# Kernel optimization log

Measured on AMD Instinct MI355X. Metric: run time of the kernel, lower is better.

The kernel has to match this reference:

```python
import jax, jax.numpy as jnp
import numpy as np

TAU = 2.0      # spikingjelly LIF default membrane time constant
VTH = 1.0      # threshold
SCALE = 0.25
NUM_HEADS = 16
EPS = 1e-5


def lif(x):
    # single-step LIF from rest (v=0, v_reset=0): u = v + (x - v)/tau = x/tau; spike = H(u - vth)
    return (x / TAU >= VTH).astype(x.dtype)


def bn(z, gamma, beta, mean, var):
    # inference-mode BatchNorm1d over channel dim of (TB, C, N)
    inv = gamma / jnp.sqrt(var + EPS)
    return z * inv[:, None] + (beta - mean * inv)[:, None]


def branch(z, w, gamma, beta, mean, var):
    # conv1x1 (pointwise channel mix) -> BN -> LIF
    z = jnp.einsum('oc,bcn->bon', w, z)
    return lif(bn(z, gamma, beta, mean, var))


def setup_inputs() -> dict:
    key = jax.random.key(0)
    ks = jax.random.split(key, 8)
    T, B, C, N = 4, 2, 512, 512
    x = jax.random.normal(ks[0], (T, B, C, N), dtype=jnp.float32)
    y = jax.random.normal(ks[1], (T, B, C, N), dtype=jnp.float32)
    def conv_w(k):
        return jax.random.normal(k, (C, C), dtype=jnp.float32) / np.float32(np.sqrt(C))
    def bn_params(k):
        km, kv = jax.random.split(k)
        gamma = jnp.full((C,), 2.0, dtype=jnp.float32)  # scale so LIF spikes are non-trivially sparse
        beta = jnp.zeros((C,), dtype=jnp.float32)
        mean = 0.1 * jax.random.normal(km, (C,), dtype=jnp.float32)
        var = 0.5 + jax.random.uniform(kv, (C,), dtype=jnp.float32)
        return gamma, beta, mean, var
    q_g, q_b, q_m, q_v = bn_params(ks[2])
    k_g, k_b, k_m, k_v = bn_params(ks[3])
    v_g, v_b, v_m, v_v = bn_params(ks[4])
    p_g, p_b, p_m, p_v = bn_params(ks[5])
    return {
        'x': x, 'y': y,
        'q_w': conv_w(jax.random.fold_in(key, 10)), 'q_g': q_g, 'q_b': q_b, 'q_m': q_m, 'q_v': q_v,
        'k_w': conv_w(jax.random.fold_in(key, 11)), 'k_g': k_g, 'k_b': k_b, 'k_m': k_m, 'k_v': k_v,
        'v_w': conv_w(jax.random.fold_in(key, 12)), 'v_g': v_g, 'v_b': v_b, 'v_m': v_m, 'v_v': v_v,
        'p_w': conv_w(jax.random.fold_in(key, 13)), 'p_g': p_g, 'p_b': p_b, 'p_m': p_m, 'p_v': p_v,
    }


def reference(x, y, q_w, q_g, q_b, q_m, q_v, k_w, k_g, k_b, k_m, k_v,
              v_w, v_g, v_b, v_m, v_v, p_w, p_g, p_b, p_m, p_v):
    T, B, C, N = x.shape
    H = NUM_HEADS
    D = C // H
    xq = x.reshape(T * B, C, N)
    yk = y.reshape(T * B, C, N)
    # q/k/v: conv1x1 + BN + LIF, then split heads: (T,B,C,N) -> (T,B,H,N,D)
    q = branch(xq, q_w, q_g, q_b, q_m, q_v).reshape(T, B, H, D, N).transpose(0, 1, 2, 4, 3)
    k = branch(yk, k_w, k_g, k_b, k_m, k_v).reshape(T, B, H, D, N).transpose(0, 1, 2, 4, 3)
    v = branch(yk, v_w, v_g, v_b, v_m, v_v).reshape(T, B, H, D, N).transpose(0, 1, 2, 4, 3)
    # softmax-free spiking attention: (Q K^T) V * scale
    attn = jnp.einsum('tbhnd,tbhmd->tbhnm', q, k)
    o = jnp.einsum('tbhnm,tbhmd->tbhnd', attn, v) * SCALE
    o = o.transpose(0, 1, 2, 4, 3).reshape(T, B, C, N)  # (T,B,H,D,N) -> (T,B,C,N)
    o = lif(o.reshape(T * B, C, N))
    o = branch(o, p_w, p_g, p_b, p_m, p_v).reshape(T, B, C, N)
    return o
```

## Files before the change

kernel.cpp:

```cpp
#include <hip/hip_runtime.h>
#include <math.h>

#define TBD 8
#define CD  512
#define ND  512
#define PLANE (TBD*CD*ND)
#define WPL   (CD*CD)

typedef unsigned short u16;
typedef unsigned int u32;
typedef _Float16 f16;
typedef __attribute__((ext_vector_type(8))) short bf16x8;
typedef __attribute__((ext_vector_type(8))) _Float16 f16x8;
typedef __attribute__((ext_vector_type(4))) float f32x4;

__device__ __forceinline__ float b2f(u16 u){
  union{u32 i; float f;} x; x.i = ((u32)u) << 16; return x.f;
}
__device__ __forceinline__ u16 f2b(float f){
  u32 u = __builtin_bit_cast(u32, f);
  u += 0x7fffu + ((u >> 16) & 1u);
  return (u16)(u >> 16);
}
__device__ __forceinline__ void async_ld16(const void* g, void* l){
  __builtin_amdgcn_global_load_lds((const __attribute__((address_space(1))) u32*)g,
      (__attribute__((address_space(3))) u32*)l, 16, 0, 0);
}

__global__ __launch_bounds__(256) void prep(
    const float* __restrict__ x, const float* __restrict__ y,
    const float* __restrict__ Qw, const float* __restrict__ Kw,
    const float* __restrict__ Vw, const float* __restrict__ Pw,
    const float* __restrict__ Qg, const float* __restrict__ Qb, const float* __restrict__ Qm, const float* __restrict__ Qv,
    const float* __restrict__ Kg, const float* __restrict__ Kb, const float* __restrict__ Km, const float* __restrict__ Kv,
    const float* __restrict__ Vg, const float* __restrict__ Vb, const float* __restrict__ Vm, const float* __restrict__ Vv,
    const float* __restrict__ Pg, const float* __restrict__ Pb, const float* __restrict__ Pm, const float* __restrict__ Pv,
    u16* __restrict__ wsu, float* __restrict__ ib)
{
  const int bx = blockIdx.x, t = threadIdx.x;
  if (bx < 1024) {
    __shared__ __align__(16) float tl[64][68];
    const int inp = bx >> 9, rem = bx & 511;
    const int tb = rem >> 6, tile = rem & 63;
    const int ct = (tile & 7) << 6, nt = (tile >> 3) << 6;
    const float* xg = inp ? y : x;
    #pragma unroll
    for (int r = 0; r < 4; ++r) {
      const int row = (t >> 4) + (r << 4);
      const int col = (t & 15) << 2;
      *(float4*)&tl[row][col] =
          *(const float4*)(xg + ((size_t)(tb*CD + ct + row))*ND + nt + col);
    }
    __syncthreads();
    const int nl = t >> 2, cb = (t & 3) << 4;
    __align__(16) u16 h[3][16];
    #pragma unroll
    for (int j = 0; j < 16; ++j) {
      const float f = tl[cb + j][nl];
      const u16 a = f2b(f);  const float r1 = f - b2f(a);
      const u16 b = f2b(r1); const float r2 = r1 - b2f(b);
      h[0][j] = a; h[1][j] = b; h[2][j] = f2b(r2);
    }
    u16* base = wsu + (size_t)inp*3*PLANE;
    const size_t rowo = ((size_t)tb*ND + nt + nl)*CD + ct + cb;
    #pragma unroll
    for (int s = 0; s < 3; ++s) {
      *(uint4*)(base + (size_t)s*PLANE + rowo)     = *(uint4*)&h[s][0];
      *(uint4*)(base + (size_t)s*PLANE + rowo + 8) = *(uint4*)&h[s][8];
    }
  } else if (bx < 2048) {
    const int b2 = bx - 1024;
    const int mat = b2 >> 8, rr = b2 & 255;
    const float* Wg = (mat==0)?Qw:(mat==1)?Kw:(mat==2)?Vw:Pw;
    const int row = (rr << 1) + (t >> 7);
    const int col = (t & 127) << 2;
    const float4 w = *(const float4*)(Wg + (size_t)row*CD + col);
    const float f[4] = {w.x, w.y, w.z, w.w};
    __align__(8) u16 h[3][4];
    #pragma unroll
    for (int j = 0; j < 4; ++j) {
      const u16 a = f2b(f[j]);  const float r1 = f[j] - b2f(a);
      const u16 b = f2b(r1);    const float r2 = r1 - b2f(b);
      h[0][j] = a; h[1][j] = b; h[2][j] = f2b(r2);
    }
    u16* base = wsu + (size_t)6*PLANE + (size_t)mat*3*WPL;
    #pragma unroll
    for (int s = 0; s < 3; ++s)
      *(uint2*)(base + (size_t)s*WPL + (size_t)row*CD + col) = *(uint2*)&h[s][0];
  } else {
    const int idx = (bx - 2048)*256 + t;
    const int br = idx >> 9, ch = idx & 511;
    const float* G = (br==0)?Qg:(br==1)?Kg:(br==2)?Vg:Pg;
    const float* B = (br==0)?Qb:(br==1)?Kb:(br==2)?Vb:Pb;
    const float* M = (br==0)?Qm:(br==1)?Km:(br==2)?Vm:Pm;
    const float* V = (br==0)?Qv:(br==1)?Kv:(br==2)?Vv:Pv;
    const float inv = G[ch] / sqrtf(V[ch] + 1e-5f);
    ib[br*1024 + ch]       = inv;
    ib[br*1024 + 512 + ch] = B[ch] - M[ch]*inv;
  }
}

template<int XS>
__global__ __launch_bounds__(256) void gemm_mfma(
    const u16* __restrict__ Ab, const u16* __restrict__ Bbp,
    const float* __restrict__ ibp,
    u16* __restrict__ qt, u16* __restrict__ spk, float* __restrict__ outf)
{
  const int bx  = blockIdx.x;
  const int idx = bx & 511;
  const int br  = bx >> 9;
  const int tb  = idx & 7;
  const int o0  = ((idx >> 3) & 7) << 6;
  const int n0  = (idx >> 6) << 6;
  const int t    = threadIdx.x;
  const int lane = t & 63, wave = t >> 6;

  const u16* A = Ab + (size_t)br*3*WPL;
  const u16* B = Bbp + (size_t)(br ? 3 : 0)*PLANE;
  const float* IB = ibp + br*1024;

  __shared__ __align__(16) u16 smem[2*3*4*512 + 2*XS*4*512];
  u16* Al = smem;
  u16* Bl = smem + 2*3*4*512;

  const int lr = lane >> 2;
  const int lc = ((lane & 3) ^ ((lane >> 3) & 3)) << 3;
  constexpr int TPW = (12 + 4*XS) / 4;

  auto stage = [&](int buf, int c0) {
    #pragma unroll
    for (int j = 0; j < TPW; ++j) {
      const int tix = wave*TPW + j;
      if (tix < 12) {
        const int s = tix >> 2, ot = tix & 3;
        async_ld16(A + (size_t)s*WPL + (size_t)(o0 + (ot<<4) + lr)*CD + c0 + lc,
                   Al + (((buf*3 + s)*4 + ot) << 9) + (lane << 3));
      } else {
        const int k = tix - 12, s = k >> 2, nt = k & 3;
        async_ld16(B + (size_t)s*PLANE + ((size_t)tb*ND + n0 + (nt<<4) + lr)*CD + c0 + lc,
                   Bl + (((buf*XS + s)*4 + nt) << 9) + (lane << 3));
      }
    }
  };

  f32x4 acc[2][2];
  const f32x4 zero = {0.f, 0.f, 0.f, 0.f};
  acc[0][0] = zero; acc[0][1] = zero; acc[1][0] = zero; acc[1][1] = zero;

  const int otb = (wave >> 1) << 1;
  const int ntb = (wave & 1) << 1;
  const int fo = ((lane & 15) << 5) + ((((lane >> 4) ^ ((lane >> 1) & 3)) & 3) << 3);

  stage(0, 0);
  for (int i = 0; i < 16; ++i) {
    const int buf = i & 1;
    __syncthreads();
    if (i < 15) stage(buf ^ 1, (i + 1) << 5);

    bf16x8 Af[3][2], Bf[XS][2];
    #pragma unroll
    for (int s = 0; s < 3; ++s)
      #pragma unroll
      for (int oy = 0; oy < 2; ++oy)
        Af[s][oy] = *(const bf16x8*)(Al + (((buf*3 + s)*4 + otb + oy) << 9) + fo);
    #pragma unroll
    for (int s = 0; s < XS; ++s)
      #pragma unroll
      for (int nx = 0; nx < 2; ++nx)
        Bf[s][nx] = *(const bf16x8*)(Bl + (((buf*XS + s)*4 + ntb + nx) << 9) + fo);

    auto mm = [&](int sa, int sb) {
      #pragma unroll
      for (int oy = 0; oy < 2; ++oy)
        #pragma unroll
        for (int nx = 0; nx < 2; ++nx)
          acc[oy][nx] = __builtin_amdgcn_mfma_f32_16x16x32_bf16(
              Af[sa][oy], Bf[sb][nx], acc[oy][nx], 0, 0, 0);
    };
    if constexpr (XS == 3) {
      mm(0,0); mm(0,1); mm(1,0); mm(1,1); mm(0,2); mm(2,0);
    } else {
      mm(0,0); mm(1,0); mm(2,0);
    }
  }

  __syncthreads();
  const int rbase = (lane >> 4) << 2;
  const int cl = lane & 15;

  if constexpr (XS == 1) {
    float* Fb = (float*)smem;
    #pragma unroll
    for (int oy = 0; oy < 2; ++oy)
      #pragma unroll
      for (int r = 0; r < 4; ++r) {
        const int chl = ((otb + oy) << 4) + rbase + r;
        const int ch = o0 + chl;
        const float inv = IB[ch], bias = IB[512 + ch];
        #pragma unroll
        for (int nx = 0; nx < 2; ++nx) {
          const bool sp = (acc[oy][nx][r] * inv + bias >= 2.0f);
          Fb[chl*68 + ((ntb + nx) << 4) + cl] = sp ? 1.0f : 0.0f;
        }
      }
    __syncthreads();
    const int row = t >> 2, seg = (t & 3) << 4;
    float* dst = outf + ((size_t)tb*CD + o0 + row)*ND + n0 + seg;
    #pragma unroll
    for (int u = 0; u < 4; ++u)
      *(float4*)(dst + 4*u) = *(float4*)&Fb[row*68 + seg + 4*u];
  } else {
    u16* Sb = smem;
    #pragma unroll
    for (int oy = 0; oy < 2; ++oy)
      #pragma unroll
      for (int r = 0; r < 4; ++r) {
        const int chl = ((otb + oy) << 4) + rbase + r;
        const int ch = o0 + chl;
        const float inv = IB[ch], bias = IB[512 + ch];
        #pragma unroll
        for (int nx = 0; nx < 2; ++nx) {
          const bool sp = (acc[oy][nx][r] * inv + bias >= 2.0f);
          Sb[chl*136 + ((ntb + nx) << 4) + cl] = sp ? (u16)0x3C00 : (u16)0;
        }
      }
    __syncthreads();
    if (br == 0) {
      const int nr = t >> 2, cs = (t & 3) << 4;
      __align__(16) u16 h[16];
      #pragma unroll
      for (int j = 0; j < 16; ++j) h[j] = Sb[(cs + j)*136 + nr];
      u16* dst = qt + ((size_t)tb*ND + n0 + nr)*CD + o0 + cs;
      *(uint4*)dst       = *(uint4*)&h[0];
      *(uint4*)(dst + 8) = *(uint4*)&h[8];
    } else {
      u16* sp_ = spk + (size_t)(br - 1)*PLANE;
      const int row = t >> 2, seg = (t & 3) << 4;
      u16* dst = sp_ + ((size_t)tb*CD + o0 + row)*ND + n0 + seg;
      *(uint4*)dst       = *(uint4*)&Sb[row*136 + seg];
      *(uint4*)(dst + 8) = *(uint4*)&Sb[row*136 + seg + 8];
    }
  }
}

__global__ __launch_bounds__(256) void attn(
    const u16* __restrict__ Qt, const u16* __restrict__ Ks,
    const u16* __restrict__ Vs, u16* __restrict__ S2T)
{
  const int tbh = blockIdx.x >> 2;
  const int n0  = (blockIdx.x & 3) << 7;
  const int t = threadIdx.x, lane = t & 63, wave = t >> 6;
  const int tb = tbh >> 4, h = tbh & 15;

  __shared__ __align__(16) u16 Kt[2*8*512];
  __shared__ __align__(16) u16 Vt[2*8*512];
  __shared__ __align__(16) u16 QTs[8*512];
  __shared__ __align__(16) u16 Gt[4*32*40];
  __shared__ __align__(16) u16 Sb[128*40];

  const u16* Kh = Ks + (size_t)tbh*32*ND;
  const u16* Vh = Vs + (size_t)tbh*32*ND;

  const int lr = lane >> 2;
  const int lc = ((lane & 3) ^ ((lane >> 3) & 3)) << 3;
  const int fo = ((lane & 15) << 5) + ((((lane >> 4) ^ ((lane >> 1) & 3)) & 3) << 3);

  f32x4 g[2][2];
  const f32x4 zero = {0.f, 0.f, 0.f, 0.f};
  g[0][0] = zero; g[0][1] = zero; g[1][0] = zero; g[1][1] = zero;

  for (int half = 0; half < 2; ++half) {
    if (half) __syncthreads();
    #pragma unroll
    for (int j = 0; j < 8; ++j) {
      const int u = wave*8 + j;
      const int mat = u >> 4, dt = (u >> 3) & 1, kc = u & 7;
      const u16* src = (mat ? Vh : Kh) + (size_t)((dt << 4) + lr)*ND + (half << 8) + (kc << 5) + lc;
      u16* dst = (mat ? Vt : Kt) + (((dt << 3) + kc) << 9) + (lane << 3);
      async_ld16(src, dst);
    }
    if (half == 0) {
      #pragma unroll
      for (int j = 0; j < 2; ++j) {
        const int nt = wave*2 + j;
        async_ld16(Qt + ((size_t)tb*ND + n0 + (nt << 4) + lr)*CD + (h << 5) + lc,
                   QTs + (nt << 9) + (lane << 3));
      }
    }
    __syncthreads();
    for (int kc = 0; kc < 8; ++kc) {
      const f16* kt = (const f16*)Kt;
      const f16* vt = (const f16*)Vt;
      f16x8 ka0 = *(const f16x8*)(kt + (kc << 9) + fo);
      f16x8 ka1 = *(const f16x8*)(kt + ((8 + kc) << 9) + fo);
      f16x8 vb0 = *(const f16x8*)(vt + (kc << 9) + fo);
      f16x8 vb1 = *(const f16x8*)(vt + ((8 + kc) << 9) + fo);
      g[0][0] = __builtin_amdgcn_mfma_f32_16x16x32_f16(ka0, vb0, g[0][0], 0,0,0);
      g[0][1] = __builtin_amdgcn_mfma_f32_16x16x32_f16(ka0, vb1, g[0][1], 0,0,0);
      g[1][0] = __builtin_amdgcn_mfma_f32_16x16x32_f16(ka1, vb0, g[1][0], 0,0,0);
      g[1][1] = __builtin_amdgcn_mfma_f32_16x16x32_f16(ka1, vb1, g[1][1], 0,0,0);
    }
  }

  f16* myG = (f16*)(Gt + wave*(32*40));
  const int rq = (lane >> 4) << 2, cl = lane & 15;
  #pragma unroll
  for (int d1t = 0; d1t < 2; ++d1t)
    #pragma unroll
    for (int d2t = 0; d2t < 2; ++d2t)
      #pragma unroll
      for (int r = 0; r < 4; ++r) {
        const int d1 = (d1t << 4) + rq + r;
        const int d2 = (d2t << 4) + cl;
        myG[d2*40 + d1] = (f16)g[d1t][d2t][r];
      }
  asm volatile("s_waitcnt lgkmcnt(0)" ::: "memory");

  f32x4 o[2][2];
  o[0][0] = zero; o[0][1] = zero; o[1][0] = zero; o[1][1] = zero;
  const f16* qs = (const f16*)QTs;
  #pragma unroll
  for (int dd = 0; dd < 2; ++dd) {
    f16x8 ga = *(const f16x8*)(myG + (((dd << 4) + cl)*40) + ((lane >> 4) << 3));
    #pragma unroll
    for (int ntl = 0; ntl < 2; ++ntl) {
      f16x8 qb = *(const f16x8*)(qs + ((wave*2 + ntl) << 9) + fo);
      o[dd][ntl] = __builtin_amdgcn_mfma_f32_16x16x32_f16(ga, qb, o[dd][ntl], 0,0,0);
    }
  }

  #pragma unroll
  for (int dd = 0; dd < 2; ++dd)
    #pragma unroll
    for (int ntl = 0; ntl < 2; ++ntl)
      #pragma unroll
      for (int r = 0; r < 4; ++r) {
        const int n_local = ((wave*2 + ntl) << 4) + cl;
        const int c_local = (dd << 4) + rq + r;
        Sb[n_local*40 + c_local] = (o[dd][ntl][r] >= 8.0f) ? (u16)0x3F80 : (u16)0;
      }
  asm volatile("s_waitcnt lgkmcnt(0)" ::: "memory");

  const int nr = (wave << 5) + (lane >> 1);
  const int cs = (lane & 1) << 4;
  u16* dst = S2T + ((size_t)tb*ND + n0 + nr)*CD + (h << 5) + cs;
  *(uint4*)dst       = *(uint4*)&Sb[nr*40 + cs];
  *(uint4*)(dst + 8) = *(uint4*)&Sb[nr*40 + cs + 8];
}

extern "C" void kernel_launch(void* const* d_in, const int* in_sizes, int n_in,
                              void* d_out, int out_size, void* d_ws, size_t ws_size,
                              hipStream_t stream)
{
  const float* x  = (const float*)d_in[0];
  const float* y  = (const float*)d_in[1];
  const float* qw = (const float*)d_in[2];
  const float* qg = (const float*)d_in[3];
  const float* qb = (const float*)d_in[4];
  const float* qm = (const float*)d_in[5];
  const float* qv = (const float*)d_in[6];
  const float* kw = (const float*)d_in[7];
  const float* kg = (const float*)d_in[8];
  const float* kb = (const float*)d_in[9];
  const float* km = (const float*)d_in[10];
  const float* kv = (const float*)d_in[11];
  const float* vw = (const float*)d_in[12];
  const float* vg = (const float*)d_in[13];
  const float* vb = (const float*)d_in[14];
  const float* vm = (const float*)d_in[15];
  const float* vv = (const float*)d_in[16];
  const float* pw = (const float*)d_in[17];
  const float* pg = (const float*)d_in[18];
  const float* pb = (const float*)d_in[19];
  const float* pm = (const float*)d_in[20];
  const float* pv = (const float*)d_in[21];

  u16* wsu = (u16*)d_ws;
  u16* Wq   = wsu + (size_t)6*PLANE;
  u16* QT   = wsu + (size_t)6*PLANE + 12*WPL;
  u16* Kspk = QT + (size_t)PLANE;
  u16* S2T  = QT + (size_t)3*PLANE;
  float* ib = (float*)(QT + (size_t)4*PLANE);

  prep<<<2056, 256, 0, stream>>>(x, y, qw, kw, vw, pw,
      qg, qb, qm, qv, kg, kb, km, kv, vg, vb, vm, vv, pg, pb, pm, pv,
      wsu, ib);

  gemm_mfma<3><<<1536, 256, 0, stream>>>(Wq, wsu, ib, QT, Kspk, nullptr);

  attn<<<512, 256, 0, stream>>>(QT, Kspk, Kspk + (size_t)PLANE, S2T);

  gemm_mfma<1><<<512, 256, 0, stream>>>(Wq + (size_t)9*WPL, S2T,
      ib + 3*1024, nullptr, nullptr, (float*)d_out);
}
```

Before: 175.5 us.

## Store GEMM spikes directly from registers and read Q untransposed in attention

The GEMM epilogue no longer stages results through shared memory before coalesced stores. Each thread now writes its spike values straight to global memory, which drops two barriers and the LDS round trip but produces scattered 2- or 4-byte stores. Q is now kept in the same channel-major layout as K and V, so its transposed write path goes away. The attention kernel instead gathers Q fragments element by element from a padded LDS tile.

```diff
diff --git a/kernel.cpp b/kernel.cpp
--- a/kernel.cpp
+++ b/kernel.cpp
@@ -104,7 +104,7 @@
 __global__ __launch_bounds__(256) void gemm_mfma(
     const u16* __restrict__ Ab, const u16* __restrict__ Bbp,
     const float* __restrict__ ibp,
-    u16* __restrict__ qt, u16* __restrict__ spk, float* __restrict__ outf)
+    u16* __restrict__ spk, float* __restrict__ outf)
 {
   const int bx  = blockIdx.x;
   const int idx = bx & 511;
@@ -184,67 +184,29 @@
     }
   }
 
-  __syncthreads();
   const int rbase = (lane >> 4) << 2;
   const int cl = lane & 15;
-
-  if constexpr (XS == 1) {
-    float* Fb = (float*)smem;
-    #pragma unroll
-    for (int oy = 0; oy < 2; ++oy)
-      #pragma unroll
-      for (int r = 0; r < 4; ++r) {
-        const int chl = ((otb + oy) << 4) + rbase + r;
-        const int ch = o0 + chl;
-        const float inv = IB[ch], bias = IB[512 + ch];
-        #pragma unroll
-        for (int nx = 0; nx < 2; ++nx) {
-          const bool sp = (acc[oy][nx][r] * inv + bias >= 2.0f);
-          Fb[chl*68 + ((ntb + nx) << 4) + cl] = sp ? 1.0f : 0.0f;
-        }
-      }
-    __syncthreads();
-    const int row = t >> 2, seg = (t & 3) << 4;
-    float* dst = outf + ((size_t)tb*CD + o0 + row)*ND + n0 + seg;
-    #pragma unroll
-    for (int u = 0; u < 4; ++u)
-      *(float4*)(dst + 4*u) = *(float4*)&Fb[row*68 + seg + 4*u];
-  } else {
-    u16* Sb = smem;
-    #pragma unroll
-    for (int oy = 0; oy < 2; ++oy)
-      #pragma unroll
-      for (int r = 0; r < 4; ++r) {
-        const int chl = ((otb + oy) << 4) + rbase + r;
-        const int ch = o0 + chl;
-        const float inv = IB[ch], bias = IB[512 + ch];
-        #pragma unroll
-        for (int nx = 0; nx < 2; ++nx) {
-          const bool sp = (acc[oy][nx][r] * inv + bias >= 2.0f);
-          Sb[chl*136 + ((ntb + nx) << 4) + cl] = sp ? (u16)0x3C00 : (u16)0;
-        }
-      }
-    __syncthreads();
-    if (br == 0) {
-      const int nr = t >> 2, cs = (t & 3) << 4;
-      __align__(16) u16 h[16];
-      #pragma unroll
-      for (int j = 0; j < 16; ++j) h[j] = Sb[(cs + j)*136 + nr];
-      u16* dst = qt + ((size_t)tb*ND + n0 + nr)*CD + o0 + cs;
-      *(uint4*)dst       = *(uint4*)&h[0];
-      *(uint4*)(dst + 8) = *(uint4*)&h[8];
-    } else {
-      u16* sp_ = spk + (size_t)(br - 1)*PLANE;
-      const int row = t >> 2, seg = (t & 3) << 4;
-      u16* dst = sp_ + ((size_t)tb*CD + o0 + row)*ND + n0 + seg;
-      *(uint4*)dst       = *(uint4*)&Sb[row*136 + seg];
-      *(uint4*)(dst + 8) = *(uint4*)&Sb[row*136 + seg + 8];
+  #pragma unroll
+  for (int oy = 0; oy < 2; ++oy) {
+    #pragma unroll
+    for (int r = 0; r < 4; ++r) {
+      const int ch = o0 + ((otb + oy) << 4) + rbase + r;
+      const float inv  = IB[ch];
+      const float bias = IB[512 + ch];
+      #pragma unroll
+      for (int nx = 0; nx < 2; ++nx) {
+        const bool sp = (acc[oy][nx][r] * inv + bias >= 2.0f);
+        const int n = n0 + ((ntb + nx) << 4) + cl;
+        const size_t off = ((size_t)tb*CD + ch)*ND + n;
+        if constexpr (XS == 1) outf[off] = sp ? 1.0f : 0.0f;
+        else spk[(size_t)br*PLANE + off] = sp ? (u16)0x3C00 : (u16)0;
+      }
     }
   }
 }
 
 __global__ __launch_bounds__(256) void attn(
-    const u16* __restrict__ Qt, const u16* __restrict__ Ks,
+    const u16* __restrict__ Qs, const u16* __restrict__ Ks,
     const u16* __restrict__ Vs, u16* __restrict__ S2T)
 {
   const int tbh = blockIdx.x >> 2;
@@ -254,12 +216,13 @@
 
   __shared__ __align__(16) u16 Kt[2*8*512];
   __shared__ __align__(16) u16 Vt[2*8*512];
-  __shared__ __align__(16) u16 QTs[8*512];
+  __shared__ __align__(16) u16 Qg[8*520];
   __shared__ __align__(16) u16 Gt[4*32*40];
   __shared__ __align__(16) u16 Sb[128*40];
 
   const u16* Kh = Ks + (size_t)tbh*32*ND;
   const u16* Vh = Vs + (size_t)tbh*32*ND;
+  const u16* Qh = Qs + (size_t)tbh*32*ND;
 
   const int lr = lane >> 2;
   const int lc = ((lane & 3) ^ ((lane >> 3) & 3)) << 3;
@@ -282,9 +245,9 @@
     if (half == 0) {
       #pragma unroll
       for (int j = 0; j < 2; ++j) {
-        const int nt = wave*2 + j;
-        async_ld16(Qt + ((size_t)tb*ND + n0 + (nt << 4) + lr)*CD + (h << 5) + lc,
-                   QTs + (nt << 9) + (lane << 3));
+        const int gq = wave*2 + j;
+        async_ld16(Qh + (size_t)((gq << 2) + (lane >> 4))*ND + n0 + ((lane & 15) << 3),
+                   Qg + gq*520 + (lane << 3));
       }
     }
     __syncthreads();
@@ -318,13 +281,18 @@
 
   f32x4 o[2][2];
   o[0][0] = zero; o[0][1] = zero; o[1][0] = zero; o[1][1] = zero;
-  const f16* qs = (const f16*)QTs;
+  const f16* ql = (const f16*)Qg;
+  const int kg = lane >> 4, n16 = lane & 15;
   #pragma unroll
-  for (int dd = 0; dd < 2; ++dd) {
-    f16x8 ga = *(const f16x8*)(myG + (((dd << 4) + cl)*40) + ((lane >> 4) << 3));
-    #pragma unroll
-    for (int ntl = 0; ntl < 2; ++ntl) {
-      f16x8 qb = *(const f16x8*)(qs + ((wave*2 + ntl) << 9) + fo);
+  for (int ntl = 0; ntl < 2; ++ntl) {
+    const int n0w = ((wave << 1) + ntl) << 4;
+    f16x8 qb;
+    #pragma unroll
+    for (int j = 0; j < 8; ++j)
+      qb[j] = ql[(2*kg + (j >> 2))*520 + (j & 3)*128 + n0w + n16];
+    #pragma unroll
+    for (int dd = 0; dd < 2; ++dd) {
+      f16x8 ga = *(const f16x8*)(myG + (((dd << 4) + cl)*40) + (kg << 3));
       o[dd][ntl] = __builtin_amdgcn_mfma_f32_16x16x32_f16(ga, qb, o[dd][ntl], 0,0,0);
     }
   }
@@ -377,19 +345,18 @@
 
   u16* wsu = (u16*)d_ws;
   u16* Wq   = wsu + (size_t)6*PLANE;
-  u16* QT   = wsu + (size_t)6*PLANE + 12*WPL;
-  u16* Kspk = QT + (size_t)PLANE;
-  u16* S2T  = QT + (size_t)3*PLANE;
-  float* ib = (float*)(QT + (size_t)4*PLANE);
+  u16* SPK  = wsu + (size_t)6*PLANE + 12*WPL;
+  u16* S2T  = SPK + (size_t)3*PLANE;
+  float* ib = (float*)(SPK + (size_t)4*PLANE);
 
   prep<<<2056, 256, 0, stream>>>(x, y, qw, kw, vw, pw,
       qg, qb, qm, qv, kg, kb, km, kv, vg, vb, vm, vv, pg, pb, pm, pv,
       wsu, ib);
 
-  gemm_mfma<3><<<1536, 256, 0, stream>>>(Wq, wsu, ib, QT, Kspk, nullptr);
-
-  attn<<<512, 256, 0, stream>>>(QT, Kspk, Kspk + (size_t)PLANE, S2T);
+  gemm_mfma<3><<<1536, 256, 0, stream>>>(Wq, wsu, ib, SPK, nullptr);
+
+  attn<<<512, 256, 0, stream>>>(SPK, SPK + (size_t)PLANE, SPK + 2*(size_t)PLANE, S2T);
 
   gemm_mfma<1><<<512, 256, 0, stream>>>(Wq + (size_t)9*WPL, S2T,
-      ib + 3*1024, nullptr, nullptr, (float*)d_out);
-}
+      ib + 3*1024, nullptr, (float*)d_out);
+}
```

Measured after the change: 170.8 us. -2.7%, faster.
